# Performance work log

Measured on AMD Instinct MI355X. Metric: run time of the kernel, lower is better.

Reference implementation:

```python
import jax, jax.numpy as jnp
from jax import lax
import numpy as np


def _conv2d(x, w, b, pad):
    # x: [N,C,H,W], w: [O,I,kh,kw] (torch OIHW layout)
    y = lax.conv_general_dilated(
        x, w, window_strides=(1, 1), padding=[(pad, pad), (pad, pad)],
        dimension_numbers=("NCHW", "OIHW", "NCHW"))
    return y + b[None, :, None, None]


def _upsample_depth(depth, mask, ratio=2):
    # depth: [N,H,W], mask: [N, 9*ratio*ratio, H, W]
    N, H, W = depth.shape
    m = mask.reshape(N, 9, ratio, ratio, H, W)
    m = jax.nn.softmax(m, axis=1)  # softmax over the 9 taps
    # 3x3 unfold with padding=1, torch F.unfold ordering: (ky, kx) row-major
    padded = jnp.pad(depth, ((0, 0), (1, 1), (1, 1)))
    patches = jnp.stack(
        [padded[:, ky:ky + H, kx:kx + W] for ky in range(3) for kx in range(3)],
        axis=1)  # [N,9,H,W]
    # weighted sum over taps, then interleave: (N,1,a,b,H,W) -> permute(0,1,4,2,5,3)
    up = jnp.einsum("nkabhw,nkhw->nhawb", m, patches)  # [N,H,a,W,b]
    return up.reshape(N, ratio * H, ratio * W)


def setup_inputs() -> dict:
    key = jax.random.key(0)
    ks = jax.random.split(key, 6)
    N, H, W = 4, 512, 640
    in_ch = 8
    depth = jax.random.normal(ks[0], (N, H, W), dtype=jnp.float32)
    cost_volume = jax.random.normal(ks[1], (N, 1, in_ch, H, W), dtype=jnp.float32)
    s1 = 1.0 / np.sqrt(in_ch * 9)
    conv1_w = jax.random.uniform(ks[2], (in_ch, in_ch, 3, 3), jnp.float32, -s1, s1)
    conv1_b = jax.random.uniform(ks[3], (in_ch,), jnp.float32, -s1, s1)
    s2 = 1.0 / np.sqrt(in_ch)
    conv2_w = jax.random.uniform(ks[4], (36, in_ch, 1, 1), jnp.float32, -s2, s2)
    conv2_b = jax.random.uniform(ks[5], (36,), jnp.float32, -s2, s2)
    return {"depth": depth, "cost_volume": cost_volume,
            "conv1_w": conv1_w, "conv1_b": conv1_b,
            "conv2_w": conv2_w, "conv2_b": conv2_b}


def reference(depth, cost_volume, conv1_w, conv1_b, conv2_w, conv2_b):
    b, c, d, h, w = cost_volume.shape
    x = cost_volume.reshape(b, c * d, h, w)
    x = jax.nn.relu(_conv2d(x, conv1_w, conv1_b, pad=1))
    mask = 0.25 * _conv2d(x, conv2_w, conv2_b, pad=0)
    return _upsample_depth(depth, mask, ratio=2)
```

## Files before the change

kernel.cpp:

```cpp
#include <hip/hip_runtime.h>

typedef _Float16 half8  __attribute__((ext_vector_type(8)));
typedef __fp16   fp16x2 __attribute__((ext_vector_type(2)));
typedef float    float4_t __attribute__((ext_vector_type(4)));

#define SH 4
#define SW 160
#define CW (SW + 2)
#define NR (SH + 2)
#define DW (CW + 1)

template <int CTRL>
__device__ __forceinline__ float rr_add(float v) {
    const int i = __float_as_int(v);
    const int p = __builtin_amdgcn_update_dpp(i, i, CTRL, 0xF, 0xF, false);
    return v + __int_as_float(p);
}
#define ROR4 0x124
#define ROR8 0x128

__global__ __launch_bounds__(256, 4) void depth_up_fused(
    const float* __restrict__ depth,
    const float* __restrict__ cv,
    const float* __restrict__ w1,
    const float* __restrict__ b1,
    const float* __restrict__ w2,
    const float* __restrict__ b2,
    float* __restrict__ out)
{
    const int H = 512, W = 640;
    const size_t HW = (size_t)H * W;
    const int n  = blockIdx.z;
    const int h0 = blockIdx.y * SH;
    const int cb = blockIdx.x * SW;
    const int tid  = threadIdx.x;
    const int lane = tid & 63;
    const int wv   = tid >> 6;
    const int o    = lane & 15;
    const int krow = lane >> 4;
    const int u    = o >> 2;
    const int q    = o & 3;

    __shared__ half8 s_cv[NR * CW];
    __shared__ float s_d[NR * DW];

    const float* __restrict__ cvn = cv + (size_t)n * 8 * HW;
    const float* __restrict__ dn  = depth + (size_t)n * HW;

    #pragma unroll
    for (int j = 0; j < 4; ++j) {
        const int i0 = tid + 256 * j;
        const int it = i0 < (NR * CW - 1) ? i0 : (NR * CW - 1);
        const int r  = it / CW;
        const int c  = it - r * CW;
        const int gh = h0 + r - 1;
        const int gw = cb + c - 1;
        const int ghs = gh < 0 ? 0 : (gh > H - 1 ? H - 1 : gh);
        const int gws = gw < 0 ? 0 : (gw > W - 1 ? W - 1 : gw);
        const bool ok = (gh == ghs) & (gw == gws);
        const float* p = cvn + (size_t)ghs * W + gws;
        float f[9];
        #pragma unroll
        for (int ch = 0; ch < 8; ++ch) f[ch] = p[(size_t)ch * HW];
        f[8] = dn[(size_t)ghs * W + gws];
        #pragma unroll
        for (int k = 0; k < 9; ++k) f[k] = ok ? f[k] : 0.0f;
        union { half8 v8; fp16x2 h2[4]; } hu;
        #pragma unroll
        for (int pq = 0; pq < 4; ++pq)
            hu.h2[pq] = __builtin_amdgcn_cvt_pkrtz(f[2 * pq], f[2 * pq + 1]);
        s_cv[r * CW + c] = hu.v8;
        s_d[r * DW + c]  = f[8];
    }

    half8 a1a[3], a1b[3];
    #pragma unroll
    for (int ki = 0; ki < 3; ++ki) {
        const int tap = 4 * ki + krow;
        #pragma unroll
        for (int j = 0; j < 8; ++j) {
            a1a[ki][j] = (tap < 9 && o < 4) ? (_Float16)w1[(o * 8 + j) * 9 + tap]
                                            : (_Float16)0.0f;
            a1b[ki][j] = (tap < 9 && o < 4) ? (_Float16)w1[((o + 4) * 8 + j) * 9 + tap]
                                            : (_Float16)0.0f;
        }
    }
    int aoff[3];
    #pragma unroll
    for (int ki = 0; ki < 3; ++ki) {
        const int tap0 = 4 * ki + krow;
        const int tap  = tap0 > 8 ? 8 : tap0;
        const int ky   = tap / 3;
        const int kx   = tap - 3 * ky;
        aoff[ki] = ((wv + ky) * CW + o + kx) * 16;
    }
    const float4_t b1a = *reinterpret_cast<const float4_t*>(b1);
    const float4_t b1b = *reinterpret_cast<const float4_t*>(b1 + 4);

    half8 b2f[3] = {};
    if (krow == 0) {
        #pragma unroll
        for (int t = 0; t < 3; ++t) {
            const int m = (o + 16 * t) > 35 ? 35 : (o + 16 * t);
            const float4_t wlo = *reinterpret_cast<const float4_t*>(w2 + m * 8);
            const float4_t whi = *reinterpret_cast<const float4_t*>(w2 + m * 8 + 4);
            #pragma unroll
            for (int j = 0; j < 4; ++j) {
                b2f[t][j]     = (_Float16)wlo[j];
                b2f[t][4 + j] = (_Float16)whi[j];
            }
        }
    }
    const float C = 0.25f * 1.44269504f;
    float b2q[3];
    #pragma unroll
    for (int t = 0; t < 3; ++t) {
        const int m = (o + 16 * t) > 35 ? 35 : (o + 16 * t);
        b2q[t] = C * b2[m];
    }
    if (u != 0) b2q[2] = -1.0e38f;

    int poff[3];
    {
        const int taps[3] = {u, u + 4, 8};
        #pragma unroll
        for (int t = 0; t < 3; ++t) {
            const int ky = taps[t] / 3;
            const int kx = taps[t] - 3 * ky;
            poff[t] = ((wv + ky) * DW + kx) * 4;
        }
    }

    __syncthreads();

    const char* cvb = (const char*)s_cv;
    const char* sdb = (const char*)s_d;
    const float4_t zero4 = {0.0f, 0.0f, 0.0f, 0.0f};

    const half8* bb0 = (const half8*)(cvb + aoff[0]);
    const half8* bb1 = (const half8*)(cvb + aoff[1]);
    const half8* bb2 = (const half8*)(cvb + aoff[2]);
    const float* pb0 = (const float*)(sdb + poff[0] + krow * 16);
    const float* pb1 = (const float*)(sdb + poff[1] + krow * 16);
    const float* pb2 = (const float*)(sdb + poff[2] + krow * 16);
    float* ob = out + ((size_t)n * 1024 + (size_t)(2 * (h0 + wv) + (q >> 1))) * 1280
                    + (size_t)(2 * (cb + 4 * krow + u) + (q & 1));

    half8 c0 = bb0[0], c1 = bb1[0], c2 = bb2[0];
    float pt0[4], pt1[4], pt2[4];
    #pragma unroll
    for (int r = 0; r < 4; ++r) {
        pt0[r] = pb0[r]; pt1[r] = pb1[r]; pt2[r] = pb2[r];
    }

    #pragma unroll 2
    for (int pp = 0; pp < SW / 16; ++pp) {
        const int np = (pp + 1 < SW / 16) ? pp + 1 : pp;
        half8 nc0 = bb0[np * 16], nc1 = bb1[np * 16], nc2 = bb2[np * 16];
        float n0[4], n1[4], n2[4];
        #pragma unroll
        for (int r = 0; r < 4; ++r) {
            n0[r] = pb0[np * 16 + r];
            n1[r] = pb1[np * 16 + r];
            n2[r] = pb2[np * 16 + r];
        }

        float4_t accA = zero4, accB = zero4;
        accA = __builtin_amdgcn_mfma_f32_16x16x32_f16(a1a[0], c0, accA, 0, 0, 0);
        accB = __builtin_amdgcn_mfma_f32_16x16x32_f16(a1b[0], c0, accB, 0, 0, 0);
        accA = __builtin_amdgcn_mfma_f32_16x16x32_f16(a1a[1], c1, accA, 0, 0, 0);
        accB = __builtin_amdgcn_mfma_f32_16x16x32_f16(a1b[1], c1, accB, 0, 0, 0);
        accA = __builtin_amdgcn_mfma_f32_16x16x32_f16(a1a[2], c2, accA, 0, 0, 0);
        accB = __builtin_amdgcn_mfma_f32_16x16x32_f16(a1b[2], c2, accB, 0, 0, 0);

        union { half8 v; fp16x2 h2[4]; } a2;
        a2.h2[0] = __builtin_amdgcn_cvt_pkrtz(fmaxf(accA[0] + b1a[0], 0.0f),
                                              fmaxf(accA[1] + b1a[1], 0.0f));
        a2.h2[1] = __builtin_amdgcn_cvt_pkrtz(fmaxf(accA[2] + b1a[2], 0.0f),
                                              fmaxf(accA[3] + b1a[3], 0.0f));
        a2.h2[2] = __builtin_amdgcn_cvt_pkrtz(fmaxf(accB[0] + b1b[0], 0.0f),
                                              fmaxf(accB[1] + b1b[1], 0.0f));
        a2.h2[3] = __builtin_amdgcn_cvt_pkrtz(fmaxf(accB[2] + b1b[2], 0.0f),
                                              fmaxf(accB[3] + b1b[3], 0.0f));

        const float4_t d2_0 = __builtin_amdgcn_mfma_f32_16x16x32_f16(a2.v, b2f[0], zero4, 0, 0, 0);
        const float4_t d2_1 = __builtin_amdgcn_mfma_f32_16x16x32_f16(a2.v, b2f[1], zero4, 0, 0, 0);
        const float4_t d2_2 = __builtin_amdgcn_mfma_f32_16x16x32_f16(a2.v, b2f[2], zero4, 0, 0, 0);

        float se[4], sp[4];
        #pragma unroll
        for (int r = 0; r < 4; ++r) {
            const float e0 = __builtin_amdgcn_exp2f(fmaf(d2_0[r], C, b2q[0]));
            const float e1 = __builtin_amdgcn_exp2f(fmaf(d2_1[r], C, b2q[1]));
            const float e2 = __builtin_amdgcn_exp2f(fmaf(d2_2[r], C, b2q[2]));
            se[r] = e0 + e1 + e2;
            sp[r] = e0 * pt0[r] + e1 * pt1[r] + e2 * pt2[r];
        }
        #pragma unroll
        for (int r = 0; r < 4; ++r) {
            se[r] = rr_add<ROR8>(rr_add<ROR4>(se[r]));
            sp[r] = rr_add<ROR8>(rr_add<ROR4>(sp[r]));
        }

        float res[4];
        #pragma unroll
        for (int r = 0; r < 4; ++r) res[r] = sp[r] * __builtin_amdgcn_rcpf(se[r]);

        const float v01 = (u & 1) ? res[1] : res[0];
        const float v23 = (u & 1) ? res[3] : res[2];
        const float val = (u & 2) ? v23 : v01;
        ob[pp * 32] = val;

        c0 = nc0; c1 = nc1; c2 = nc2;
        #pragma unroll
        for (int r = 0; r < 4; ++r) {
            pt0[r] = n0[r]; pt1[r] = n1[r]; pt2[r] = n2[r];
        }
    }
}

extern "C" void kernel_launch(void* const* d_in, const int* in_sizes, int n_in,
                              void* d_out, int out_size, void* d_ws, size_t ws_size,
                              hipStream_t stream) {
    (void)in_sizes; (void)n_in; (void)out_size; (void)d_ws; (void)ws_size;
    const float* depth = (const float*)d_in[0];
    const float* cv    = (const float*)d_in[1];
    const float* w1    = (const float*)d_in[2];
    const float* b1    = (const float*)d_in[3];
    const float* w2    = (const float*)d_in[4];
    const float* b2    = (const float*)d_in[5];
    float* out = (float*)d_out;

    dim3 grid(640 / SW, 512 / SH, 4);
    dim3 block(256);
    hipLaunchKernelGGL(depth_up_fused, grid, block, 0, stream,
                       depth, cv, w1, b1, w2, b2, out);
}
```

Before: 48.02 us.

## Process two row tiles per block with prefetch into double-buffered shared memory

Measured after the change: 45.00 us. 6.3% less time.

```diff
diff --git a/kernel.cpp b/kernel.cpp
--- a/kernel.cpp
+++ b/kernel.cpp
@@ -4,11 +4,11 @@
 typedef __fp16   fp16x2 __attribute__((ext_vector_type(2)));
 typedef float    float4_t __attribute__((ext_vector_type(4)));
 
-#define SH 4
 #define SW 160
 #define CW (SW + 2)
-#define NR (SH + 2)
+#define NR 6
 #define DW (CW + 1)
+#define NITEM (NR * CW)
 
 template <int CTRL>
 __device__ __forceinline__ float rr_add(float v) {
@@ -31,7 +31,7 @@
     const int H = 512, W = 640;
     const size_t HW = (size_t)H * W;
     const int n  = blockIdx.z;
-    const int h0 = blockIdx.y * SH;
+    const int h0 = blockIdx.y * 8;
     const int cb = blockIdx.x * SW;
     const int tid  = threadIdx.x;
     const int lane = tid & 63;
@@ -41,8 +41,8 @@
     const int u    = o >> 2;
     const int q    = o & 3;
 
-    __shared__ half8 s_cv[NR * CW];
-    __shared__ float s_d[NR * DW];
+    __shared__ half8 s_cv[2][NITEM];
+    __shared__ float s_d[2][NR * DW];
 
     const float* __restrict__ cvn = cv + (size_t)n * 8 * HW;
     const float* __restrict__ dn  = depth + (size_t)n * HW;
@@ -50,7 +50,7 @@
     #pragma unroll
     for (int j = 0; j < 4; ++j) {
         const int i0 = tid + 256 * j;
-        const int it = i0 < (NR * CW - 1) ? i0 : (NR * CW - 1);
+        const int it = i0 < (NITEM - 1) ? i0 : (NITEM - 1);
         const int r  = it / CW;
         const int c  = it - r * CW;
         const int gh = h0 + r - 1;
@@ -69,8 +69,8 @@
         #pragma unroll
         for (int pq = 0; pq < 4; ++pq)
             hu.h2[pq] = __builtin_amdgcn_cvt_pkrtz(f[2 * pq], f[2 * pq + 1]);
-        s_cv[r * CW + c] = hu.v8;
-        s_d[r * DW + c]  = f[8];
+        s_cv[0][r * CW + c] = hu.v8;
+        s_d[0][r * DW + c]  = f[8];
     }
 
     half8 a1a[3], a1b[3];
@@ -131,92 +131,116 @@
         }
     }
 
+    float rf[4][9];
+    #pragma unroll
+    for (int j = 0; j < 4; ++j) {
+        const int i0 = tid + 256 * j;
+        const int it = i0 < (NITEM - 1) ? i0 : (NITEM - 1);
+        const int r  = it / CW;
+        const int c  = it - r * CW;
+        const int gh = h0 + 4 + r - 1;
+        const int gw = cb + c - 1;
+        const int ghs = gh < 0 ? 0 : (gh > H - 1 ? H - 1 : gh);
+        const int gws = gw < 0 ? 0 : (gw > W - 1 ? W - 1 : gw);
+        const float* p = cvn + (size_t)ghs * W + gws;
+        #pragma unroll
+        for (int ch = 0; ch < 8; ++ch) rf[j][ch] = p[(size_t)ch * HW];
+        rf[j][8] = dn[(size_t)ghs * W + gws];
+    }
+    __builtin_amdgcn_sched_barrier(0);
     __syncthreads();
 
-    const char* cvb = (const char*)s_cv;
-    const char* sdb = (const char*)s_d;
     const float4_t zero4 = {0.0f, 0.0f, 0.0f, 0.0f};
 
-    const half8* bb0 = (const half8*)(cvb + aoff[0]);
-    const half8* bb1 = (const half8*)(cvb + aoff[1]);
-    const half8* bb2 = (const half8*)(cvb + aoff[2]);
-    const float* pb0 = (const float*)(sdb + poff[0] + krow * 16);
-    const float* pb1 = (const float*)(sdb + poff[1] + krow * 16);
-    const float* pb2 = (const float*)(sdb + poff[2] + krow * 16);
-    float* ob = out + ((size_t)n * 1024 + (size_t)(2 * (h0 + wv) + (q >> 1))) * 1280
-                    + (size_t)(2 * (cb + 4 * krow + u) + (q & 1));
-
-    half8 c0 = bb0[0], c1 = bb1[0], c2 = bb2[0];
-    float pt0[4], pt1[4], pt2[4];
-    #pragma unroll
-    for (int r = 0; r < 4; ++r) {
-        pt0[r] = pb0[r]; pt1[r] = pb1[r]; pt2[r] = pb2[r];
-    }
-
-    #pragma unroll 2
-    for (int pp = 0; pp < SW / 16; ++pp) {
-        const int np = (pp + 1 < SW / 16) ? pp + 1 : pp;
-        half8 nc0 = bb0[np * 16], nc1 = bb1[np * 16], nc2 = bb2[np * 16];
-        float n0[4], n1[4], n2[4];
-        #pragma unroll
-        for (int r = 0; r < 4; ++r) {
-            n0[r] = pb0[np * 16 + r];
-            n1[r] = pb1[np * 16 + r];
-            n2[r] = pb2[np * 16 + r];
-        }
-
-        float4_t accA = zero4, accB = zero4;
-        accA = __builtin_amdgcn_mfma_f32_16x16x32_f16(a1a[0], c0, accA, 0, 0, 0);
-        accB = __builtin_amdgcn_mfma_f32_16x16x32_f16(a1b[0], c0, accB, 0, 0, 0);
-        accA = __builtin_amdgcn_mfma_f32_16x16x32_f16(a1a[1], c1, accA, 0, 0, 0);
-        accB = __builtin_amdgcn_mfma_f32_16x16x32_f16(a1b[1], c1, accB, 0, 0, 0);
-        accA = __builtin_amdgcn_mfma_f32_16x16x32_f16(a1a[2], c2, accA, 0, 0, 0);
-        accB = __builtin_amdgcn_mfma_f32_16x16x32_f16(a1b[2], c2, accB, 0, 0, 0);
-
-        union { half8 v; fp16x2 h2[4]; } a2;
-        a2.h2[0] = __builtin_amdgcn_cvt_pkrtz(fmaxf(accA[0] + b1a[0], 0.0f),
-                                              fmaxf(accA[1] + b1a[1], 0.0f));
-        a2.h2[1] = __builtin_amdgcn_cvt_pkrtz(fmaxf(accA[2] + b1a[2], 0.0f),
-                                              fmaxf(accA[3] + b1a[3], 0.0f));
-        a2.h2[2] = __builtin_amdgcn_cvt_pkrtz(fmaxf(accB[0] + b1b[0], 0.0f),
-                                              fmaxf(accB[1] + b1b[1], 0.0f));
-        a2.h2[3] = __builtin_amdgcn_cvt_pkrtz(fmaxf(accB[2] + b1b[2], 0.0f),
-                                              fmaxf(accB[3] + b1b[3], 0.0f));
-
-        const float4_t d2_0 = __builtin_amdgcn_mfma_f32_16x16x32_f16(a2.v, b2f[0], zero4, 0, 0, 0);
-        const float4_t d2_1 = __builtin_amdgcn_mfma_f32_16x16x32_f16(a2.v, b2f[1], zero4, 0, 0, 0);
-        const float4_t d2_2 = __builtin_amdgcn_mfma_f32_16x16x32_f16(a2.v, b2f[2], zero4, 0, 0, 0);
-
-        float se[4], sp[4];
-        #pragma unroll
-        for (int r = 0; r < 4; ++r) {
-            const float e0 = __builtin_amdgcn_exp2f(fmaf(d2_0[r], C, b2q[0]));
-            const float e1 = __builtin_amdgcn_exp2f(fmaf(d2_1[r], C, b2q[1]));
-            const float e2 = __builtin_amdgcn_exp2f(fmaf(d2_2[r], C, b2q[2]));
-            se[r] = e0 + e1 + e2;
-            sp[r] = e0 * pt0[r] + e1 * pt1[r] + e2 * pt2[r];
-        }
-        #pragma unroll
-        for (int r = 0; r < 4; ++r) {
-            se[r] = rr_add<ROR8>(rr_add<ROR4>(se[r]));
-            sp[r] = rr_add<ROR8>(rr_add<ROR4>(sp[r]));
-        }
-
-        float res[4];
-        #pragma unroll
-        for (int r = 0; r < 4; ++r) res[r] = sp[r] * __builtin_amdgcn_rcpf(se[r]);
-
-        const float v01 = (u & 1) ? res[1] : res[0];
-        const float v23 = (u & 1) ? res[3] : res[2];
-        const float val = (u & 2) ? v23 : v01;
-        ob[pp * 32] = val;
-
-        c0 = nc0; c1 = nc1; c2 = nc2;
-        #pragma unroll
-        for (int r = 0; r < 4; ++r) {
-            pt0[r] = n0[r]; pt1[r] = n1[r]; pt2[r] = n2[r];
-        }
-    }
+    auto compute = [&](const char* cvb, const char* sdb, float* obp)
+        __attribute__((always_inline)) {
+        const half8* bb0 = (const half8*)(cvb + aoff[0]);
+        const half8* bb1 = (const half8*)(cvb + aoff[1]);
+        const half8* bb2 = (const half8*)(cvb + aoff[2]);
+        const float* pb0 = (const float*)(sdb + poff[0] + krow * 16);
+        const float* pb1 = (const float*)(sdb + poff[1] + krow * 16);
+        const float* pb2 = (const float*)(sdb + poff[2] + krow * 16);
+        #pragma unroll 2
+        for (int pp = 0; pp < SW / 16; ++pp) {
+            const half8 c0 = bb0[pp * 16];
+            const half8 c1 = bb1[pp * 16];
+            const half8 c2 = bb2[pp * 16];
+
+            float4_t accA = zero4, accB = zero4;
+            accA = __builtin_amdgcn_mfma_f32_16x16x32_f16(a1a[0], c0, accA, 0, 0, 0);
+            accB = __builtin_amdgcn_mfma_f32_16x16x32_f16(a1b[0], c0, accB, 0, 0, 0);
+            accA = __builtin_amdgcn_mfma_f32_16x16x32_f16(a1a[1], c1, accA, 0, 0, 0);
+            accB = __builtin_amdgcn_mfma_f32_16x16x32_f16(a1b[1], c1, accB, 0, 0, 0);
+            accA = __builtin_amdgcn_mfma_f32_16x16x32_f16(a1a[2], c2, accA, 0, 0, 0);
+            accB = __builtin_amdgcn_mfma_f32_16x16x32_f16(a1b[2], c2, accB, 0, 0, 0);
+
+            union { half8 v; fp16x2 h2[4]; } a2;
+            a2.h2[0] = __builtin_amdgcn_cvt_pkrtz(fmaxf(accA[0] + b1a[0], 0.0f),
+                                                  fmaxf(accA[1] + b1a[1], 0.0f));
+            a2.h2[1] = __builtin_amdgcn_cvt_pkrtz(fmaxf(accA[2] + b1a[2], 0.0f),
+                                                  fmaxf(accA[3] + b1a[3], 0.0f));
+            a2.h2[2] = __builtin_amdgcn_cvt_pkrtz(fmaxf(accB[0] + b1b[0], 0.0f),
+                                                  fmaxf(accB[1] + b1b[1], 0.0f));
+            a2.h2[3] = __builtin_amdgcn_cvt_pkrtz(fmaxf(accB[2] + b1b[2], 0.0f),
+                                                  fmaxf(accB[3] + b1b[3], 0.0f));
+
+            const float4_t d2_0 = __builtin_amdgcn_mfma_f32_16x16x32_f16(a2.v, b2f[0], zero4, 0, 0, 0);
+            const float4_t d2_1 = __builtin_amdgcn_mfma_f32_16x16x32_f16(a2.v, b2f[1], zero4, 0, 0, 0);
+            const float4_t d2_2 = __builtin_amdgcn_mfma_f32_16x16x32_f16(a2.v, b2f[2], zero4, 0, 0, 0);
+
+            float se[4], sp[4];
+            #pragma unroll
+            for (int r = 0; r < 4; ++r) {
+                const float e0 = __builtin_amdgcn_exp2f(fmaf(d2_0[r], C, b2q[0]));
+                const float e1 = __builtin_amdgcn_exp2f(fmaf(d2_1[r], C, b2q[1]));
+                const float e2 = __builtin_amdgcn_exp2f(fmaf(d2_2[r], C, b2q[2]));
+                se[r] = e0 + e1 + e2;
+                sp[r] = e0 * pb0[pp * 16 + r] + e1 * pb1[pp * 16 + r]
+                      + e2 * pb2[pp * 16 + r];
+            }
+            #pragma unroll
+            for (int r = 0; r < 4; ++r) {
+                se[r] = rr_add<ROR8>(rr_add<ROR4>(se[r]));
+                sp[r] = rr_add<ROR8>(rr_add<ROR4>(sp[r]));
+            }
+            float res[4];
+            #pragma unroll
+            for (int r = 0; r < 4; ++r) res[r] = sp[r] * __builtin_amdgcn_rcpf(se[r]);
+            const float v01 = (u & 1) ? res[1] : res[0];
+            const float v23 = (u & 1) ? res[3] : res[2];
+            obp[pp * 32] = (u & 2) ? v23 : v01;
+        }
+    };
+
+    float* ob0 = out + ((size_t)n * 1024 + (size_t)(2 * (h0 + wv) + (q >> 1))) * 1280
+                     + (size_t)(2 * (cb + 4 * krow + u) + (q & 1));
+
+    compute((const char*)&s_cv[0][0], (const char*)&s_d[0][0], ob0);
+
+    #pragma unroll
+    for (int j = 0; j < 4; ++j) {
+        const int i0 = tid + 256 * j;
+        const int it = i0 < (NITEM - 1) ? i0 : (NITEM - 1);
+        const int r  = it / CW;
+        const int c  = it - r * CW;
+        const int gh = h0 + 4 + r - 1;
+        const int gw = cb + c - 1;
+        const int ghs = gh < 0 ? 0 : (gh > H - 1 ? H - 1 : gh);
+        const int gws = gw < 0 ? 0 : (gw > W - 1 ? W - 1 : gw);
+        const bool ok = (gh == ghs) & (gw == gws);
+        float f[9];
+        #pragma unroll
+        for (int k = 0; k < 9; ++k) f[k] = ok ? rf[j][k] : 0.0f;
+        union { half8 v8; fp16x2 h2[4]; } hu;
+        #pragma unroll
+        for (int pq = 0; pq < 4; ++pq)
+            hu.h2[pq] = __builtin_amdgcn_cvt_pkrtz(f[2 * pq], f[2 * pq + 1]);
+        s_cv[1][r * CW + c] = hu.v8;
+        s_d[1][r * DW + c]  = f[8];
+    }
+    __syncthreads();
+
+    compute((const char*)&s_cv[1][0], (const char*)&s_d[1][0], ob0 + 8 * 1280);
 }
 
 extern "C" void kernel_launch(void* const* d_in, const int* in_sizes, int n_in,
@@ -231,7 +255,7 @@
     const float* b2    = (const float*)d_in[5];
     float* out = (float*)d_out;
 
-    dim3 grid(640 / SW, 512 / SH, 4);
+    dim3 grid(640 / SW, 512 / 8, 4);
     dim3 block(256);
     hipLaunchKernelGGL(depth_up_fused, grid, block, 0, stream,
                        depth, cv, w1, b1, w2, b2, out);
```
